# Kernel optimization log

Hardware: AMD Instinct MI355X
Metric: run time of the kernel (lower is better)

The kernel has to match this reference:

```python
import jax, jax.numpy as jnp
import numpy as np

B, D, L, T, NC, PS = 32, 768, 12, 197, 1000, 16  # batch, embed, layers, tokens(196+cls), classes, patch
EPS = 1e-5


def setup_inputs() -> dict:
    key = jax.random.key(0)
    ks = iter(jax.random.split(key, 40))

    def w(*shape):
        return (jax.random.normal(next(ks), shape, dtype=jnp.float32) * 0.02)

    inp = {
        "x": jax.random.normal(next(ks), (B, 1, 14, 14, PS, PS), dtype=jnp.float32),
        "cls": w(1, 1, D),
        "emb_w": w(PS * PS, D), "emb_b": jnp.zeros((D,), jnp.float32),
        "pos": w(T, D),
        # stacked per-layer params, leading dim L
        "Wq": w(L, D, D), "bq": jnp.zeros((L, D), jnp.float32),
        "Wk": w(L, D, D), "bk": jnp.zeros((L, D), jnp.float32),
        "Wv": w(L, D, D), "bv": jnp.zeros((L, D), jnp.float32),
        "Wo": w(L, D, D), "bo": jnp.zeros((L, D), jnp.float32),
        "g1": jnp.ones((L, D), jnp.float32), "be1": jnp.zeros((L, D), jnp.float32),
        "W1": w(L, D, D), "b1": jnp.zeros((L, D), jnp.float32),
        "W2": w(L, D, D), "b2": jnp.zeros((L, D), jnp.float32),
        "g2": jnp.ones((L, D), jnp.float32), "be2": jnp.zeros((L, D), jnp.float32),
        "fg": jnp.ones((D,), jnp.float32), "fb": jnp.zeros((D,), jnp.float32),
        "head_w": w(D, NC), "head_b": jnp.zeros((NC,), jnp.float32),
    }
    return inp


def _layernorm(x, g, b):
    m = jnp.mean(x, axis=-1, keepdims=True)
    v = jnp.mean((x - m) ** 2, axis=-1, keepdims=True)
    return (x - m) * jax.lax.rsqrt(v + EPS) * g + b


def _forward(x, cls, emb_w, emb_b, pos, Wq, bq, Wk, bk, Wv, bv, Wo, bo,
             g1, be1, W1, b1, W2, b2, g2, be2, fg, fb, head_w, head_b):
    b = x.shape[0]
    # (b,1,nh,nw,ph,pw) -> (b, nh*nw, ph*pw)
    patches = x.reshape(b, 14 * 14, PS * PS)
    pch = patches @ emb_w + emb_b                       # [b,196,D]
    hdn = jnp.concatenate([jnp.broadcast_to(cls, (b, 1, D)), pch], axis=1)
    hdn = hdn + pos                                     # [b,T,D]
    scale = D ** (-0.5)                                 # note: full dim, single-head

    def layer(h, p):
        (wq, bq_, wk, bk_, wv, bv_, wo, bo_, g1_, be1_, w1, b1_, w2, b2_, g2_, be2_) = p
        q = h @ wq + bq_
        k = h @ wk + bk_
        v = h @ wv + bv_
        att = jax.nn.softmax(jnp.einsum("btd,bsd->bts", q, k) * scale, axis=-1)
        out = jnp.einsum("bts,bsd->btd", att, v) @ wo + bo_
        h = _layernorm(h + out, g1_, be1_)
        f = jax.nn.gelu(h @ w1 + b1_, approximate=False) @ w2 + b2_
        h = _layernorm(h + f, g2_, be2_)
        return h, None

    params = (Wq, bq, Wk, bk, Wv, bv, Wo, bo, g1, be1, W1, b1, W2, b2, g2, be2)
    hdn, _ = jax.lax.scan(layer, hdn, params)
    out = _layernorm(hdn[:, 0, :], fg, fb)
    return out @ head_w + head_b                        # [b,NC]


def reference(x, cls, emb_w, emb_b, pos, Wq, bq, Wk, bk, Wv, bv, Wo, bo,
              g1, be1, W1, b1, W2, b2, g2, be2, fg, fb, head_w, head_b):
    return _forward(x, cls, emb_w, emb_b, pos, Wq, bq, Wk, bk, Wv, bv, Wo, bo,
                    g1, be1, W1, b1, W2, b2, g2, be2, fg, fb, head_w, head_b)
```

## Files before the change

### kernel.cpp

```cpp
#include <hip/hip_runtime.h>
#include <hip/hip_bf16.h>
#include <math.h>

typedef short short8 __attribute__((ext_vector_type(8)));
typedef short short4v __attribute__((ext_vector_type(4)));
typedef float floatx4 __attribute__((ext_vector_type(4)));

#define DEV static __device__ __forceinline__

DEV float s2f(short v) {
    unsigned int u = ((unsigned int)(unsigned short)v) << 16;
    float f;
    __builtin_memcpy(&f, &u, 4);
    return f;
}
DEV short f2s(float f) {
    __hip_bfloat16 b = __float2bfloat16(f);
    short s;
    __builtin_memcpy(&s, &b, 2);
    return s;
}

DEV void async_copy16(const void* g, void* l) {
    __builtin_amdgcn_global_load_lds(
        (const __attribute__((address_space(1))) void*)g,
        (__attribute__((address_space(3))) void*)l, 16, 0, 0);
}

DEV int xcd_chunk(int id, int n) {
    const int q = n >> 3, r = n & 7;
    const int x = id & 7, j = id >> 3;
    return (x < r ? x * (q + 1) : r * (q + 1) + (x - r) * q) + j;
}

struct GP {
    const short* A;  long long zA; int lda;
    const short* Bt; long long zB; int ldb;
    const float* bias;
    const short* R;  int ldr;
    short* C;        long long zC; int ldc;
    int M, N, K;
};

template<int EPI>
DEV void gemm_body(short* smem, const GP p, int bx, int by, int bz)
{
    const short* A  = p.A  + (long long)bz * p.zA;
    const short* Bt = p.Bt + (long long)bz * p.zB;
    short* C        = p.C  + (long long)bz * p.zC;

    const int tid   = threadIdx.x;
    const int lane  = tid & 63;
    const int wave  = tid >> 6;
    const int tileM = bx * 64;
    const int tileN = by * 128;
    const int wm    = (wave & 1) * 32;
    const int wn    = (wave >> 1) * 64;

    floatx4 acc[2][4];
#pragma unroll
    for (int mt = 0; mt < 2; ++mt)
#pragma unroll
        for (int nt = 0; nt < 4; ++nt)
            acc[mt][nt] = (floatx4){0.f, 0.f, 0.f, 0.f};

    for (int k0 = 0; k0 < p.K; k0 += 64) {
#pragma unroll
        for (int h = 0; h < 2; ++h) {
            {
                const int c   = tid;
                const int row = c >> 2;
                const int ko  = (c & 3) * 8;
                async_copy16(A + (long long)(tileM + row) * p.lda + k0 + h * 32 + ko,
                             &smem[h * 2048 + c * 8]);
            }
#pragma unroll
            for (int i = 0; i < 2; ++i) {
                const int c   = i * 256 + tid;
                const int row = c >> 2;
                const int ko  = (c & 3) * 8;
                async_copy16(Bt + (long long)(tileN + row) * p.ldb + k0 + h * 32 + ko,
                             &smem[4096 + h * 4096 + c * 8]);
            }
        }
        __syncthreads();

        const int fr = lane & 15;
        const int ko = (lane >> 4) * 8;
#pragma unroll
        for (int h = 0; h < 2; ++h) {
            const short* pA = &smem[h * 2048];
            const short* pB = &smem[4096 + h * 4096];
            short8 af[2], bf[4];
#pragma unroll
            for (int t = 0; t < 2; ++t)
                af[t] = *(const short8*)&pA[(wm + fr + t * 16) * 32 + ko];
#pragma unroll
            for (int t = 0; t < 4; ++t)
                bf[t] = *(const short8*)&pB[(wn + fr + t * 16) * 32 + ko];
#pragma unroll
            for (int mt = 0; mt < 2; ++mt)
#pragma unroll
                for (int nt = 0; nt < 4; ++nt)
                    acc[mt][nt] = __builtin_amdgcn_mfma_f32_16x16x32_bf16(
                        af[mt], bf[nt], acc[mt][nt], 0, 0, 0);
        }
        __syncthreads();
    }

    float* eps = (float*)smem + wave * (16 * 68);
    const int col = lane & 15;
    const int rb  = (lane >> 4) * 4;
#pragma unroll
    for (int mt = 0; mt < 2; ++mt) {
        const int gr0 = tileM + wm + mt * 16;
        const int gc0 = tileN + wn;
#pragma unroll
        for (int nt = 0; nt < 4; ++nt) {
            float bv = 0.0f;
            if constexpr (EPI != 3) { if (p.bias) bv = p.bias[gc0 + nt * 16 + col]; }
#pragma unroll
            for (int r = 0; r < 4; ++r) {
                float v = acc[mt][nt][r] + bv;
                if constexpr (EPI == 1) v = 0.5f * v * (1.0f + erff(v * 0.70710678118654752f));
                eps[(rb + r) * 68 + nt * 16 + col] = v;
            }
        }
#pragma unroll
        for (int j = 0; j < 2; ++j) {
            const int r  = (lane >> 3) + 8 * j;
            const int cb = (lane & 7) * 8;
            const floatx4 f0 = *(const floatx4*)&eps[r * 68 + cb];
            const floatx4 f1 = *(const floatx4*)&eps[r * 68 + cb + 4];
            const int gr = gr0 + r;
            if (gr >= p.M) continue;
            float rbv = 0.0f;
            if constexpr (EPI == 3) rbv = p.bias[gr];
            short8 o;
            if constexpr (EPI == 2) {
                const short8 rr = *(const short8*)&p.R[(long long)gr * p.ldr + gc0 + cb];
#pragma unroll
                for (int i = 0; i < 4; ++i) {
                    o[i]     = f2s(f0[i] + s2f(rr[i]));
                    o[4 + i] = f2s(f1[i] + s2f(rr[4 + i]));
                }
            } else {
#pragma unroll
                for (int i = 0; i < 4; ++i) {
                    o[i]     = f2s(f0[i] + rbv);
                    o[4 + i] = f2s(f1[i] + rbv);
                }
            }
            *(short8*)&C[(long long)gr * p.ldc + gc0 + cb] = o;
        }
    }
}

template<int EPI>
__global__ __launch_bounds__(256) void gemm64_k(GP p)
{
    __shared__ short smem[12288];
    gemm_body<EPI>(smem, p, blockIdx.x, blockIdx.y, blockIdx.z);
}

template<int EPI>
DEV void gemm128_body(short* smem, const GP p, int bx, int by, int bz)
{
    const short* A  = p.A  + (long long)bz * p.zA;
    const short* Bt = p.Bt + (long long)bz * p.zB;
    short* C        = p.C  + (long long)bz * p.zC;

    const int tid   = threadIdx.x;
    const int lane  = tid & 63;
    const int wave  = tid >> 6;
    const int tileM = bx * 128;
    const int tileN = by * 128;
    const int wm    = (wave & 1) * 64;
    const int wn    = (wave >> 1) * 64;

    floatx4 acc[4][4];
#pragma unroll
    for (int mt = 0; mt < 4; ++mt)
#pragma unroll
        for (int nt = 0; nt < 4; ++nt)
            acc[mt][nt] = (floatx4){0.f, 0.f, 0.f, 0.f};

    const int arow = tid >> 3;
    const int asl  = ((tid & 7) ^ (arow & 7)) * 8;
    const short* gA = A  + (long long)(tileM + arow) * p.lda + asl;
    const short* gB = Bt + (long long)(tileN + arow) * p.ldb + asl;
    const long long stA = 32LL * p.lda;
    const long long stB = 32LL * p.ldb;

    auto stage = [&](int buf, int k0) {
        short* dst = smem + buf * 16384;
#pragma unroll
        for (int i = 0; i < 4; ++i)
            async_copy16(gA + i * stA + k0, &dst[(i * 256 + tid) * 8]);
#pragma unroll
        for (int i = 0; i < 4; ++i)
            async_copy16(gB + i * stB + k0, &dst[8192 + (i * 256 + tid) * 8]);
    };

    const int nK = p.K >> 6;
    stage(0, 0);
    __syncthreads();

    const int fr = lane & 15;
    const int q  = lane >> 4;
    for (int ks = 0; ks < nK; ++ks) {
        if (ks + 1 < nK) stage((ks + 1) & 1, (ks + 1) << 6);
        const short* pA = smem + (ks & 1) * 16384;
        const short* pB = pA + 8192;
#pragma unroll
        for (int h = 0; h < 2; ++h) {
            short8 af[4], bf[4];
#pragma unroll
            for (int t = 0; t < 4; ++t) {
                const int row = wm + t * 16 + fr;
                af[t] = *(const short8*)&pA[row * 64 + (((h * 4 + q) ^ (row & 7)) * 8)];
            }
#pragma unroll
            for (int t = 0; t < 4; ++t) {
                const int row = wn + t * 16 + fr;
                bf[t] = *(const short8*)&pB[row * 64 + (((h * 4 + q) ^ (row & 7)) * 8)];
            }
#pragma unroll
            for (int mt = 0; mt < 4; ++mt)
#pragma unroll
                for (int nt = 0; nt < 4; ++nt)
                    acc[mt][nt] = __builtin_amdgcn_mfma_f32_16x16x32_bf16(
                        af[mt], bf[nt], acc[mt][nt], 0, 0, 0);
        }
        __syncthreads();
    }

    float* eps = (float*)smem + wave * (16 * 68);
    const int col = lane & 15;
    const int rb  = (lane >> 4) * 4;
#pragma unroll
    for (int mt = 0; mt < 4; ++mt) {
        const int gr0 = tileM + wm + mt * 16;
        const int gc0 = tileN + wn;
#pragma unroll
        for (int nt = 0; nt < 4; ++nt) {
            float bv = 0.0f;
            if constexpr (EPI != 3) { if (p.bias) bv = p.bias[gc0 + nt * 16 + col]; }
#pragma unroll
            for (int r = 0; r < 4; ++r) {
                float v = acc[mt][nt][r] + bv;
                if constexpr (EPI == 1) v = 0.5f * v * (1.0f + erff(v * 0.70710678118654752f));
                eps[(rb + r) * 68 + nt * 16 + col] = v;
            }
        }
#pragma unroll
        for (int j = 0; j < 2; ++j) {
            const int r  = (lane >> 3) + 8 * j;
            const int cb = (lane & 7) * 8;
            const floatx4 f0 = *(const floatx4*)&eps[r * 68 + cb];
            const floatx4 f1 = *(const floatx4*)&eps[r * 68 + cb + 4];
            const int gr = gr0 + r;
            if (gr >= p.M) continue;
            float rbv = 0.0f;
            if constexpr (EPI == 3) rbv = p.bias[gr];
            short8 o;
            if constexpr (EPI == 2) {
                const short8 rr = *(const short8*)&p.R[(long long)gr * p.ldr + gc0 + cb];
#pragma unroll
                for (int i = 0; i < 4; ++i) {
                    o[i]     = f2s(f0[i] + s2f(rr[i]));
                    o[4 + i] = f2s(f1[i] + s2f(rr[4 + i]));
                }
            } else {
#pragma unroll
                for (int i = 0; i < 4; ++i) {
                    o[i]     = f2s(f0[i] + rbv);
                    o[4 + i] = f2s(f1[i] + rbv);
                }
            }
            *(short8*)&C[(long long)gr * p.ldc + gc0 + cb] = o;
        }
    }
}

template<int EPI>
__global__ __launch_bounds__(256) void gemm128f_k(GP p, int nBy, int perZ)
{
    __shared__ short smem[32768];
    const int pos = xcd_chunk((int)blockIdx.x, (int)gridDim.x);
    const int z   = pos / perZ;
    const int rem = pos % perZ;
    gemm128_body<EPI>(smem, p, rem / nBy, rem % nBy, z);
}

__global__ __launch_bounds__(256) void qkvt_k(GP qk, GP vt, int nQK)
{
    __shared__ short smem[32768];
    const int pos = xcd_chunk((int)blockIdx.x, (int)gridDim.x);
    if (pos < nQK) {
        gemm128_body<0>(smem, qk, pos / 12, pos % 12, 0);
    } else {
        const int i2 = pos - nQK;
        gemm128_body<3>(smem, vt, (i2 % 12) >> 1, i2 & 1, i2 / 12);
    }
}

__global__ void tconv_k(const float* __restrict__ in, short* __restrict__ out,
                        int K, int N, long long inZ, long long outZ)
{
    __shared__ float t[32][33];
    in  += (long long)blockIdx.z * inZ;
    out += (long long)blockIdx.z * outZ;
    const int n0 = blockIdx.x * 32, k0 = blockIdx.y * 32;
    const int tx = threadIdx.x, ty = threadIdx.y;
#pragma unroll
    for (int i = 0; i < 4; ++i)
        t[ty + i * 8][tx] = in[(long long)(k0 + ty + i * 8) * N + n0 + tx];
    __syncthreads();
#pragma unroll
    for (int i = 0; i < 4; ++i)
        out[(long long)(n0 + ty + i * 8) * K + k0 + tx] = f2s(t[tx][ty + i * 8]);
}

__global__ __launch_bounds__(256) void cvtx4_k(const float* __restrict__ x,
                                               short* __restrict__ xb, int n4)
{
    const int i = blockIdx.x * 256 + threadIdx.x;
    if (i >= n4) return;
    const floatx4 v = *(const floatx4*)&x[i * 4];
    short4v o;
#pragma unroll
    for (int e = 0; e < 4; ++e) o[e] = f2s(v[e]);
    *(short4v*)&xb[i * 4] = o;
}

__global__ __launch_bounds__(256) void bqk_k(
    const float* __restrict__ bq, const float* __restrict__ bk,
    float* __restrict__ out)
{
    const int i = blockIdx.x * 256 + threadIdx.x;
    if (i >= 12 * 1536) return;
    const int l = i / 1536, j = i % 1536;
    out[i] = (j < 768) ? bq[l * 768 + j] : bk[l * 768 + j - 768];
}

__global__ __launch_bounds__(256) void assemble4_k(
    const short* __restrict__ P, const float* __restrict__ cls,
    const float* __restrict__ pos, short* __restrict__ H)
{
    const int c = blockIdx.x * 256 + threadIdx.x;
    if (c >= 32 * 197 * 192) return;
    const int d4 = c % 192;
    const int t  = (c / 192) % 197;
    const long long b = c / (192 * 197);
    const floatx4 pv = *(const floatx4*)&pos[t * 768 + d4 * 4];
    float o[4];
    if (t == 0) {
        const floatx4 cv = *(const floatx4*)&cls[d4 * 4];
#pragma unroll
        for (int e = 0; e < 4; ++e) o[e] = cv[e] + pv[e];
    } else {
        const short4v pc = *(const short4v*)&P[(b * 196 + t - 1) * 768 + d4 * 4];
#pragma unroll
        for (int e = 0; e < 4; ++e) o[e] = s2f(pc[e]) + pv[e];
    }
    short4v ov;
#pragma unroll
    for (int e = 0; e < 4; ++e) ov[e] = f2s(o[e]);
    *(short4v*)&H[((b * 197 + t) * 768) + d4 * 4] = ov;
}

__global__ __launch_bounds__(256) void softmaxw_k(short* __restrict__ S, float scale)
{
    const int row  = blockIdx.x * 4 + (threadIdx.x >> 6);
    const int lane = threadIdx.x & 63;
    if (row >= 32 * 197) return;
    const int b = row / 197, t = row % 197;
    short* s = S + ((long long)b * 256 + t) * 256;
    const int c0 = lane * 4;

    const short4v v = *(const short4v*)&s[c0];
    float f[4], mx = -1e30f;
#pragma unroll
    for (int e = 0; e < 4; ++e) {
        f[e] = (c0 + e < 197) ? s2f(v[e]) * scale : -1e30f;
        mx = fmaxf(mx, f[e]);
    }
#pragma unroll
    for (int m = 1; m < 64; m <<= 1) mx = fmaxf(mx, __shfl_xor(mx, m, 64));
    float e4[4], sum = 0.0f;
#pragma unroll
    for (int e = 0; e < 4; ++e) {
        e4[e] = (c0 + e < 197) ? expf(f[e] - mx) : 0.0f;
        sum += e4[e];
    }
#pragma unroll
    for (int m = 1; m < 64; m <<= 1) sum += __shfl_xor(sum, m, 64);
    const float inv = 1.0f / sum;
    short4v o;
#pragma unroll
    for (int e = 0; e < 4; ++e) o[e] = f2s(e4[e] * inv);
    *(short4v*)&s[c0] = o;
}

__global__ __launch_bounds__(256) void lnw_k(
    const short* __restrict__ X, long long xs,
    short* __restrict__ Y, long long ys,
    const float* __restrict__ g, const float* __restrict__ be, int nrows)
{
    const int row  = blockIdx.x * 4 + (threadIdx.x >> 6);
    const int lane = threadIdx.x & 63;
    if (row >= nrows) return;
    const short* x = X + (long long)row * xs;
    short* y = Y + (long long)row * ys;

    float v[12], s = 0.0f, sq = 0.0f;
#pragma unroll
    for (int j = 0; j < 3; ++j) {
        const short4v t4 = *(const short4v*)&x[(lane + 64 * j) * 4];
#pragma unroll
        for (int e = 0; e < 4; ++e) {
            const float t = s2f(t4[e]);
            v[j * 4 + e] = t; s += t; sq += t * t;
        }
    }
#pragma unroll
    for (int m = 1; m < 64; m <<= 1) {
        s  += __shfl_xor(s,  m, 64);
        sq += __shfl_xor(sq, m, 64);
    }
    const float mean = s * (1.0f / 768.0f);
    const float var  = sq * (1.0f / 768.0f) - mean * mean;
    const float rs   = rsqrtf(var + 1e-5f);
#pragma unroll
    for (int j = 0; j < 3; ++j) {
        const int d0 = (lane + 64 * j) * 4;
        const floatx4 gv = *(const floatx4*)&g[d0];
        const floatx4 bv = *(const floatx4*)&be[d0];
        short4v o;
#pragma unroll
        for (int e = 0; e < 4; ++e)
            o[e] = f2s((v[j * 4 + e] - mean) * rs * gv[e] + bv[e]);
        *(short4v*)&y[d0] = o;
    }
}

__global__ __launch_bounds__(256) void head3_k(
    const short* __restrict__ hc, const float* __restrict__ W,
    const float* __restrict__ hb, float* __restrict__ out)
{
    const int b  = blockIdx.y;
    const int cc = threadIdx.x & 63;
    const int ks = threadIdx.x >> 6;
    const int c  = blockIdx.x * 64 + cc;
    __shared__ float h[768];
    __shared__ float red[4][64];
    for (int i = threadIdx.x; i < 768; i += 256) h[i] = s2f(hc[b * 768 + i]);
    __syncthreads();
    float acc = 0.0f;
    if (c < 1000) {
        const int k0 = ks * 192;
        for (int k = k0; k < k0 + 192; ++k) acc += h[k] * W[k * 1000 + c];
    }
    red[ks][cc] = acc;
    __syncthreads();
    if (ks == 0 && c < 1000)
        out[b * 1000 + c] = red[0][cc] + red[1][cc] + red[2][cc] + red[3][cc] + hb[c];
}

extern "C" void kernel_launch(void* const* d_in, const int* in_sizes, int n_in,
                              void* d_out, int out_size, void* d_ws, size_t ws_size,
                              hipStream_t stream)
{
    const float* x     = (const float*)d_in[0];
    const float* cls   = (const float*)d_in[1];
    const float* emb_w = (const float*)d_in[2];
    const float* emb_b = (const float*)d_in[3];
    const float* pos   = (const float*)d_in[4];
    const float* Wq    = (const float*)d_in[5];
    const float* bq    = (const float*)d_in[6];
    const float* Wk    = (const float*)d_in[7];
    const float* bk    = (const float*)d_in[8];
    const float* Wv    = (const float*)d_in[9];
    const float* bv    = (const float*)d_in[10];
    const float* Wo    = (const float*)d_in[11];
    const float* bo    = (const float*)d_in[12];
    const float* g1    = (const float*)d_in[13];
    const float* be1   = (const float*)d_in[14];
    const float* W1    = (const float*)d_in[15];
    const float* b1    = (const float*)d_in[16];
    const float* W2    = (const float*)d_in[17];
    const float* b2    = (const float*)d_in[18];
    const float* g2    = (const float*)d_in[19];
    const float* be2   = (const float*)d_in[20];
    const float* fg    = (const float*)d_in[21];
    const float* fb    = (const float*)d_in[22];
    const float* hw    = (const float*)d_in[23];
    const float* hb    = (const float*)d_in[24];

    char* ws = (char*)d_ws;
    long long o = 0;
    short* WtQK = (short*)(ws + o); o += 12LL * 1536 * 768 * 2;
    short* WtV  = (short*)(ws + o); o += 12LL * 768 * 768 * 2;
    short* WtO  = (short*)(ws + o); o += 12LL * 768 * 768 * 2;
    short* Wt1  = (short*)(ws + o); o += 12LL * 768 * 768 * 2;
    short* Wt2  = (short*)(ws + o); o += 12LL * 768 * 768 * 2;
    short* embT = (short*)(ws + o); o += 768LL * 256 * 2;
    short* H    = (short*)(ws + o); o += 6400LL * 768 * 2;
    short* QKVb = (short*)(ws + o); o += 6400LL * 1536 * 2;
    short* AO   = (short*)(ws + o); o += 6400LL * 768 * 2;
    short* VT   = (short*)(ws + o); o += 32LL * 768 * 256 * 2;
    short* T1   = VT;
    short* S    = (short*)(ws + o); o += 32LL * 256 * 256 * 2;
    short* xb   = S;
    short* hc   = (short*)(ws + o); o += 64LL * 768 * 2;
    float* bqk  = (float*)(ws + o); o += 12LL * 1536 * 4;

    const dim3 blk(256);
    const dim3 tblk(32, 8);
    const float scale = 0.03608439182435161f;
    const long long sH  = 197LL * 768;
    const long long sQK = 197LL * 1536;
    const long long sS  = 256LL * 256;
    const long long sVT = 768LL * 256;

    tconv_k<<<dim3(24, 8, 1),   tblk, 0, stream>>>(emb_w, embT, 256, 768, 0, 0);
    tconv_k<<<dim3(24, 24, 12), tblk, 0, stream>>>(Wq, WtQK,             768, 768, 589824, 1536LL * 768);
    tconv_k<<<dim3(24, 24, 12), tblk, 0, stream>>>(Wk, WtQK + 768 * 768, 768, 768, 589824, 1536LL * 768);
    tconv_k<<<dim3(24, 24, 12), tblk, 0, stream>>>(Wv, WtV, 768, 768, 589824, 589824);
    tconv_k<<<dim3(24, 24, 12), tblk, 0, stream>>>(Wo, WtO, 768, 768, 589824, 589824);
    tconv_k<<<dim3(24, 24, 12), tblk, 0, stream>>>(W1, Wt1, 768, 768, 589824, 589824);
    tconv_k<<<dim3(24, 24, 12), tblk, 0, stream>>>(W2, Wt2, 768, 768, 589824, 589824);
    cvtx4_k<<<dim3(1568), blk, 0, stream>>>(x, xb, 6272 * 64);
    bqk_k<<<dim3(72), blk, 0, stream>>>(bq, bk, bqk);

    {
        GP p = { xb, 0, 256, embT, 0, 256, emb_b, nullptr, 0, T1, 0, 768, 6272, 768, 256 };
        gemm64_k<0><<<dim3(98, 6), blk, 0, stream>>>(p);
    }
    assemble4_k<<<dim3((32 * 197 * 192 + 255) / 256), blk, 0, stream>>>(T1, cls, pos, H);

    for (int l = 0; l < 12; ++l) {
        const long long w1o = (long long)l * 589824;
        const long long vo  = (long long)l * 768;
        {
            GP qk = { H, 0, 768, WtQK + (long long)l * 1536 * 768, 0, 768,
                      bqk + l * 1536, nullptr, 0, QKVb, 0, 1536, 6304, 1536, 768 };
            GP vt = { WtV + w1o, 0, 768, H, sH, 768, bv + vo,
                      nullptr, 0, VT, sVT, 256, 768, 256, 768 };
            qkvt_k<<<dim3(600 + 384), blk, 0, stream>>>(qk, vt, 600);
        }
        {
            GP p = { QKVb, sQK, 1536, QKVb + 768, sQK, 1536, nullptr,
                     nullptr, 0, S, sS, 256, 197, 256, 768 };
            gemm64_k<0><<<dim3(4, 2, 32), blk, 0, stream>>>(p);
        }
        softmaxw_k<<<dim3(1576), blk, 0, stream>>>(S, scale);
        {
            GP p = { S, sS, 256, VT, sVT, 256, nullptr,
                     nullptr, 0, AO, sH, 768, 197, 768, 256 };
            gemm128f_k<0><<<dim3(384), blk, 0, stream>>>(p, 6, 12);
        }
        {
            GP p = { AO, 0, 768, WtO + w1o, 0, 768, bo + vo, H, 768,
                     T1, 0, 768, 6304, 768, 768 };
            gemm128f_k<2><<<dim3(300), blk, 0, stream>>>(p, 6, 300);
        }
        lnw_k<<<dim3(1576), blk, 0, stream>>>(T1, 768, H, 768, g1 + vo, be1 + vo, 6304);
        {
            GP p = { H, 0, 768, Wt1 + w1o, 0, 768, b1 + vo, nullptr, 0,
                     T1, 0, 768, 6304, 768, 768 };
            gemm128f_k<1><<<dim3(300), blk, 0, stream>>>(p, 6, 300);
        }
        {
            GP p = { T1, 0, 768, Wt2 + w1o, 0, 768, b2 + vo, H, 768,
                     AO, 0, 768, 6304, 768, 768 };
            gemm128f_k<2><<<dim3(300), blk, 0, stream>>>(p, 6, 300);
        }
        lnw_k<<<dim3(1576), blk, 0, stream>>>(AO, 768, H, 768, g2 + vo, be2 + vo, 6304);
    }

    lnw_k<<<dim3(8), blk, 0, stream>>>(H, sH, hc, 768, fg, fb, 32);
    head3_k<<<dim3(16, 32), blk, 0, stream>>>(hc, hw, hb, (float*)d_out);
}
```

Before: 2.105 ms.

## Switch non-QKV GEMMs to double-buffered swizzled 64x128 tiles

```diff
diff --git a/kernel.cpp b/kernel.cpp
--- a/kernel.cpp
+++ b/kernel.cpp
@@ -43,7 +43,7 @@
 };
 
 template<int EPI>
-DEV void gemm_body(short* smem, const GP p, int bx, int by, int bz)
+DEV void gemm128_body(short* smem, const GP p, int bx, int by, int bz)
 {
     const short* A  = p.A  + (long long)bz * p.zA;
     const short* Bt = p.Bt + (long long)bz * p.zB;
@@ -52,54 +52,60 @@
     const int tid   = threadIdx.x;
     const int lane  = tid & 63;
     const int wave  = tid >> 6;
-    const int tileM = bx * 64;
+    const int tileM = bx * 128;
     const int tileN = by * 128;
-    const int wm    = (wave & 1) * 32;
+    const int wm    = (wave & 1) * 64;
     const int wn    = (wave >> 1) * 64;
 
-    floatx4 acc[2][4];
-#pragma unroll
-    for (int mt = 0; mt < 2; ++mt)
+    floatx4 acc[4][4];
+#pragma unroll
+    for (int mt = 0; mt < 4; ++mt)
 #pragma unroll
         for (int nt = 0; nt < 4; ++nt)
             acc[mt][nt] = (floatx4){0.f, 0.f, 0.f, 0.f};
 
-    for (int k0 = 0; k0 < p.K; k0 += 64) {
+    const int arow = tid >> 3;
+    const int asl  = ((tid & 7) ^ (arow & 7)) * 8;
+    const short* gA = A  + (long long)(tileM + arow) * p.lda + asl;
+    const short* gB = Bt + (long long)(tileN + arow) * p.ldb + asl;
+    const long long stA = 32LL * p.lda;
+    const long long stB = 32LL * p.ldb;
+
+    auto stage = [&](int buf, int k0) {
+        short* dst = smem + buf * 16384;
+#pragma unroll
+        for (int i = 0; i < 4; ++i)
+            async_copy16(gA + i * stA + k0, &dst[(i * 256 + tid) * 8]);
+#pragma unroll
+        for (int i = 0; i < 4; ++i)
+            async_copy16(gB + i * stB + k0, &dst[8192 + (i * 256 + tid) * 8]);
+    };
+
+    const int nK = p.K >> 6;
+    stage(0, 0);
+    __syncthreads();
+
+    const int fr = lane & 15;
+    const int q  = lane >> 4;
+    for (int ks = 0; ks < nK; ++ks) {
+        if (ks + 1 < nK) stage((ks + 1) & 1, (ks + 1) << 6);
+        const short* pA = smem + (ks & 1) * 16384;
+        const short* pB = pA + 8192;
 #pragma unroll
         for (int h = 0; h < 2; ++h) {
-            {
-                const int c   = tid;
-                const int row = c >> 2;
-                const int ko  = (c & 3) * 8;
-                async_copy16(A + (long long)(tileM + row) * p.lda + k0 + h * 32 + ko,
-                             &smem[h * 2048 + c * 8]);
-            }
-#pragma unroll
-            for (int i = 0; i < 2; ++i) {
-                const int c   = i * 256 + tid;
-                const int row = c >> 2;
-                const int ko  = (c & 3) * 8;
-                async_copy16(Bt + (long long)(tileN + row) * p.ldb + k0 + h * 32 + ko,
-                             &smem[4096 + h * 4096 + c * 8]);
-            }
-        }
-        __syncthreads();
-
-        const int fr = lane & 15;
-        const int ko = (lane >> 4) * 8;
-#pragma unroll
-        for (int h = 0; h < 2; ++h) {
-            const short* pA = &smem[h * 2048];
-            const short* pB = &smem[4096 + h * 4096];
-            short8 af[2], bf[4];
-#pragma unroll
-            for (int t = 0; t < 2; ++t)
-                af[t] = *(const short8*)&pA[(wm + fr + t * 16) * 32 + ko];
-#pragma unroll
-            for (int t = 0; t < 4; ++t)
-                bf[t] = *(const short8*)&pB[(wn + fr + t * 16) * 32 + ko];
-#pragma unroll
-            for (int mt = 0; mt < 2; ++mt)
+            short8 af[4], bf[4];
+#pragma unroll
+            for (int t = 0; t < 4; ++t) {
+                const int row = wm + t * 16 + fr;
+                af[t] = *(const short8*)&pA[row * 64 + (((h * 4 + q) ^ (row & 7)) * 8)];
+            }
+#pragma unroll
+            for (int t = 0; t < 4; ++t) {
+                const int row = wn + t * 16 + fr;
+                bf[t] = *(const short8*)&pB[row * 64 + (((h * 4 + q) ^ (row & 7)) * 8)];
+            }
+#pragma unroll
+            for (int mt = 0; mt < 4; ++mt)
 #pragma unroll
                 for (int nt = 0; nt < 4; ++nt)
                     acc[mt][nt] = __builtin_amdgcn_mfma_f32_16x16x32_bf16(
@@ -112,7 +118,7 @@
     const int col = lane & 15;
     const int rb  = (lane >> 4) * 4;
 #pragma unroll
-    for (int mt = 0; mt < 2; ++mt) {
+    for (int mt = 0; mt < 4; ++mt) {
         const int gr0 = tileM + wm + mt * 16;
         const int gc0 = tileN + wn;
 #pragma unroll
@@ -156,15 +162,20 @@
     }
 }
 
+__global__ __launch_bounds__(256) void qkvt_k(GP qk, GP vt, int nQK)
+{
+    __shared__ short smem[32768];
+    const int pos = xcd_chunk((int)blockIdx.x, (int)gridDim.x);
+    if (pos < nQK) {
+        gemm128_body<0>(smem, qk, pos / 12, pos % 12, 0);
+    } else {
+        const int i2 = pos - nQK;
+        gemm128_body<3>(smem, vt, (i2 % 12) >> 1, i2 & 1, i2 / 12);
+    }
+}
+
 template<int EPI>
-__global__ __launch_bounds__(256) void gemm64_k(GP p)
-{
-    __shared__ short smem[12288];
-    gemm_body<EPI>(smem, p, blockIdx.x, blockIdx.y, blockIdx.z);
-}
-
-template<int EPI>
-DEV void gemm128_body(short* smem, const GP p, int bx, int by, int bz)
+DEV void gemm64d_body(short* smem, const GP p, int bx, int by, int bz)
 {
     const short* A  = p.A  + (long long)bz * p.zA;
     const short* Bt = p.Bt + (long long)bz * p.zB;
@@ -173,14 +184,14 @@
     const int tid   = threadIdx.x;
     const int lane  = tid & 63;
     const int wave  = tid >> 6;
-    const int tileM = bx * 128;
+    const int tileM = bx * 64;
     const int tileN = by * 128;
-    const int wm    = (wave & 1) * 64;
+    const int wm    = (wave & 1) * 32;
     const int wn    = (wave >> 1) * 64;
 
-    floatx4 acc[4][4];
-#pragma unroll
-    for (int mt = 0; mt < 4; ++mt)
+    floatx4 acc[2][4];
+#pragma unroll
+    for (int mt = 0; mt < 2; ++mt)
 #pragma unroll
         for (int nt = 0; nt < 4; ++nt)
             acc[mt][nt] = (floatx4){0.f, 0.f, 0.f, 0.f};
@@ -193,13 +204,13 @@
     const long long stB = 32LL * p.ldb;
 
     auto stage = [&](int buf, int k0) {
-        short* dst = smem + buf * 16384;
+        short* dst = smem + buf * 12288;
+#pragma unroll
+        for (int i = 0; i < 2; ++i)
+            async_copy16(gA + i * stA + k0, &dst[(i * 256 + tid) * 8]);
 #pragma unroll
         for (int i = 0; i < 4; ++i)
-            async_copy16(gA + i * stA + k0, &dst[(i * 256 + tid) * 8]);
-#pragma unroll
-        for (int i = 0; i < 4; ++i)
-            async_copy16(gB + i * stB + k0, &dst[8192 + (i * 256 + tid) * 8]);
+            async_copy16(gB + i * stB + k0, &dst[4096 + (i * 256 + tid) * 8]);
     };
 
     const int nK = p.K >> 6;
@@ -210,13 +221,13 @@
     const int q  = lane >> 4;
     for (int ks = 0; ks < nK; ++ks) {
         if (ks + 1 < nK) stage((ks + 1) & 1, (ks + 1) << 6);
-        const short* pA = smem + (ks & 1) * 16384;
-        const short* pB = pA + 8192;
+        const short* pA = smem + (ks & 1) * 12288;
+        const short* pB = pA + 4096;
 #pragma unroll
         for (int h = 0; h < 2; ++h) {
-            short8 af[4], bf[4];
-#pragma unroll
-            for (int t = 0; t < 4; ++t) {
+            short8 af[2], bf[4];
+#pragma unroll
+            for (int t = 0; t < 2; ++t) {
                 const int row = wm + t * 16 + fr;
                 af[t] = *(const short8*)&pA[row * 64 + (((h * 4 + q) ^ (row & 7)) * 8)];
             }
@@ -226,7 +237,7 @@
                 bf[t] = *(const short8*)&pB[row * 64 + (((h * 4 + q) ^ (row & 7)) * 8)];
             }
 #pragma unroll
-            for (int mt = 0; mt < 4; ++mt)
+            for (int mt = 0; mt < 2; ++mt)
 #pragma unroll
                 for (int nt = 0; nt < 4; ++nt)
                     acc[mt][nt] = __builtin_amdgcn_mfma_f32_16x16x32_bf16(
@@ -239,13 +250,13 @@
     const int col = lane & 15;
     const int rb  = (lane >> 4) * 4;
 #pragma unroll
-    for (int mt = 0; mt < 4; ++mt) {
+    for (int mt = 0; mt < 2; ++mt) {
         const int gr0 = tileM + wm + mt * 16;
         const int gc0 = tileN + wn;
 #pragma unroll
         for (int nt = 0; nt < 4; ++nt) {
             float bv = 0.0f;
-            if constexpr (EPI != 3) { if (p.bias) bv = p.bias[gc0 + nt * 16 + col]; }
+            if (p.bias) bv = p.bias[gc0 + nt * 16 + col];
 #pragma unroll
             for (int r = 0; r < 4; ++r) {
                 float v = acc[mt][nt][r] + bv;
@@ -261,8 +272,6 @@
             const floatx4 f1 = *(const floatx4*)&eps[r * 68 + cb + 4];
             const int gr = gr0 + r;
             if (gr >= p.M) continue;
-            float rbv = 0.0f;
-            if constexpr (EPI == 3) rbv = p.bias[gr];
             short8 o;
             if constexpr (EPI == 2) {
                 const short8 rr = *(const short8*)&p.R[(long long)gr * p.ldr + gc0 + cb];
@@ -274,8 +283,8 @@
             } else {
 #pragma unroll
                 for (int i = 0; i < 4; ++i) {
-                    o[i]     = f2s(f0[i] + rbv);
-                    o[4 + i] = f2s(f1[i] + rbv);
+                    o[i]     = f2s(f0[i]);
+                    o[4 + i] = f2s(f1[i]);
                 }
             }
             *(short8*)&C[(long long)gr * p.ldc + gc0 + cb] = o;
@@ -284,25 +293,13 @@
 }
 
 template<int EPI>
-__global__ __launch_bounds__(256) void gemm128f_k(GP p, int nBy, int perZ)
-{
-    __shared__ short smem[32768];
+__global__ __launch_bounds__(256) void gemm64d_k(GP p, int nBy, int perZ)
+{
+    __shared__ short smem[24576];
     const int pos = xcd_chunk((int)blockIdx.x, (int)gridDim.x);
     const int z   = pos / perZ;
     const int rem = pos % perZ;
-    gemm128_body<EPI>(smem, p, rem / nBy, rem % nBy, z);
-}
-
-__global__ __launch_bounds__(256) void qkvt_k(GP qk, GP vt, int nQK)
-{
-    __shared__ short smem[32768];
-    const int pos = xcd_chunk((int)blockIdx.x, (int)gridDim.x);
-    if (pos < nQK) {
-        gemm128_body<0>(smem, qk, pos / 12, pos % 12, 0);
-    } else {
-        const int i2 = pos - nQK;
-        gemm128_body<3>(smem, vt, (i2 % 12) >> 1, i2 & 1, i2 / 12);
-    }
+    gemm64d_body<EPI>(smem, p, rem / nBy, rem % nBy, z);
 }
 
 __global__ void tconv_k(const float* __restrict__ in, short* __restrict__ out,
@@ -536,7 +533,7 @@
 
     {
         GP p = { xb, 0, 256, embT, 0, 256, emb_b, nullptr, 0, T1, 0, 768, 6272, 768, 256 };
-        gemm64_k<0><<<dim3(98, 6), blk, 0, stream>>>(p);
+        gemm64d_k<0><<<dim3(588), blk, 0, stream>>>(p, 6, 588);
     }
     assemble4_k<<<dim3((32 * 197 * 192 + 255) / 256), blk, 0, stream>>>(T1, cls, pos, H);
 
@@ -553,29 +550,29 @@
         {
             GP p = { QKVb, sQK, 1536, QKVb + 768, sQK, 1536, nullptr,
                      nullptr, 0, S, sS, 256, 197, 256, 768 };
-            gemm64_k<0><<<dim3(4, 2, 32), blk, 0, stream>>>(p);
+            gemm64d_k<0><<<dim3(256), blk, 0, stream>>>(p, 2, 8);
         }
         softmaxw_k<<<dim3(1576), blk, 0, stream>>>(S, scale);
         {
             GP p = { S, sS, 256, VT, sVT, 256, nullptr,
                      nullptr, 0, AO, sH, 768, 197, 768, 256 };
-            gemm128f_k<0><<<dim3(384), blk, 0, stream>>>(p, 6, 12);
+            gemm64d_k<0><<<dim3(768), blk, 0, stream>>>(p, 6, 24);
         }
         {
             GP p = { AO, 0, 768, WtO + w1o, 0, 768, bo + vo, H, 768,
                      T1, 0, 768, 6304, 768, 768 };
-            gemm128f_k<2><<<dim3(300), blk, 0, stream>>>(p, 6, 300);
+            gemm64d_k<2><<<dim3(594), blk, 0, stream>>>(p, 6, 594);
         }
         lnw_k<<<dim3(1576), blk, 0, stream>>>(T1, 768, H, 768, g1 + vo, be1 + vo, 6304);
         {
             GP p = { H, 0, 768, Wt1 + w1o, 0, 768, b1 + vo, nullptr, 0,
                      T1, 0, 768, 6304, 768, 768 };
-            gemm128f_k<1><<<dim3(300), blk, 0, stream>>>(p, 6, 300);
+            gemm64d_k<1><<<dim3(594), blk, 0, stream>>>(p, 6, 594);
         }
         {
             GP p = { T1, 0, 768, Wt2 + w1o, 0, 768, b2 + vo, H, 768,
                      AO, 0, 768, 6304, 768, 768 };
-            gemm128f_k<2><<<dim3(300), blk, 0, stream>>>(p, 6, 300);
+            gemm64d_k<2><<<dim3(594), blk, 0, stream>>>(p, 6, 594);
         }
         lnw_k<<<dim3(1576), blk, 0, stream>>>(AO, 768, H, 768, g2 + vo, be2 + vo, 6304);
     }
```

New measurement: 1.877 ms. 1.12x faster.
